# Kernel tuning notes

Measured on AMD Instinct MI355X. Metric: run time of the kernel, lower is better.

Reference implementation:

```python
import jax, jax.numpy as jnp
import numpy as np

M, N, D = 16384, 16384, 256


def setup_inputs() -> dict:
    key = jax.random.key(0)
    k1, k2, k3 = jax.random.split(key, 3)
    x = jax.random.normal(k1, (M, D), dtype=jnp.float32)
    X = jax.random.normal(k2, (N, D), dtype=jnp.float32)
    residuals = jax.random.normal(k3, (N,), dtype=jnp.float32)
    return {"x": x, "X": X, "residuals": residuals}


def reference(x, X, residuals):
    n, d = X.shape
    # Scott's rule: h = mean(std(X, unbiased)) * n^(-1/(d+4))
    h = jnp.mean(jnp.std(X, axis=0, ddof=1)) * (n ** (-1.0 / (d + 4)))
    inv_bw_sq = 1.0 / (2.0 * h * h)
    sq = (jnp.sum(x * x, axis=1)[:, None]
          + jnp.sum(X * X, axis=1)[None, :]
          - 2.0 * (x @ X.T))
    sq = jnp.maximum(sq, 0.0)
    w = jnp.exp(-sq * inv_bw_sq)                     # (m, n)
    num = w @ residuals                              # (m,)
    den = jnp.sum(w, axis=1) + 1e-8                  # (m,)
    return num / den
```

## Files before the change

kernel.cpp:

```cpp
#include <hip/hip_runtime.h>
#include <stdint.h>

#define MDIM 16384
#define NDIM 16384
#define DDIM 256
#define NSPLIT 4
#define NSTRIP 4096
#define BM 128
#define NT 32

typedef __attribute__((ext_vector_type(16))) float f32x16;
typedef __attribute__((ext_vector_type(8))) int i32x8;

#define SC1 0x7F7F7F7F

static constexpr size_t COLPART_OFF = 0;
static constexpr size_t SCAL_OFF    = 512u * 1024u;
static constexpr size_t AX_OFF      = SCAL_OFF + 1024u;
static constexpr size_t BXR_OFF     = AX_OFF + 64u * 1024u;
static constexpr size_t BXM_OFF     = BXR_OFF + 64u * 1024u;
static constexpr size_t X8_OFF      = 1ull << 20;
static constexpr size_t B8_OFF      = X8_OFF + (4ull << 20);
static constexpr size_t NUMP_OFF    = B8_OFF + (4ull << 20) + (512ull << 10);
static constexpr size_t DENP_OFF    = NUMP_OFF + (size_t)NSPLIT * MDIM * 4u;

__device__ inline unsigned short f2bf_rne(float f) {
    uint32_t u = __builtin_bit_cast(uint32_t, f);
    u += 0x7fffu + ((u >> 16) & 1u);
    return (unsigned short)(u >> 16);
}

__global__ void k1_colstats(const float* __restrict__ X, float2* __restrict__ part) {
    const int col = threadIdx.x;
    const int b   = blockIdx.x;
    const float* p = X + (size_t)b * 64 * DDIM + col;
    float s = 0.f, sq = 0.f;
#pragma unroll 8
    for (int r = 0; r < 64; ++r) {
        float v = p[(size_t)r * DDIM];
        s += v; sq += v * v;
    }
    part[b * 256 + col] = make_float2(s, sq);
}

__global__ void k2_finalize(const float2* __restrict__ part, float* __restrict__ scal) {
    const int t = threadIdx.x;
    float s = 0.f, sq = 0.f;
#pragma unroll 8
    for (int b = 0; b < 256; ++b) {
        float2 v = part[b * 256 + t];
        s += v.x; sq += v.y;
    }
    const float n = (float)NDIM;
    float var = (sq - s * s / n) / (n - 1.0f);
    float sd  = sqrtf(fmaxf(var, 0.f));
    __shared__ float red[256];
    red[t] = sd;
    __syncthreads();
    for (int o = 128; o > 0; o >>= 1) {
        if (t < o) red[t] += red[t + o];
        __syncthreads();
    }
    if (t == 0) {
        float h = (red[0] / 256.0f) * exp2f(log2f(n) * (-1.0f / (DDIM + 4.0f)));
        float c = 1.0f / (2.0f * h * h);
        scal[0] = c;
        scal[1] = sqrtf(2.0f * c);
    }
}

__global__ void k3_prep(const float* __restrict__ src,
                        unsigned char* __restrict__ dst8,
                        float* __restrict__ ax,
                        const float* __restrict__ resid, unsigned int* __restrict__ bxrp,
                        const float* __restrict__ scal) {
    const int lane = threadIdx.x & 63;
    const int wv   = threadIdx.x >> 6;
    const int row  = blockIdx.x * 4 + wv;
    const float c = scal[0], s = scal[1];
    float4 v = *((const float4*)(src + (size_t)row * DDIM) + lane);
    float nsq = v.x * v.x + v.y * v.y + v.z * v.z + v.w * v.w;
#pragma unroll
    for (int o = 1; o < 64; o <<= 1) nsq += __shfl_xor(nsq, o);

    unsigned int r8 = 0;
    r8 = __builtin_amdgcn_cvt_pk_fp8_f32(v.x * s, v.y * s, r8, 0);
    r8 = __builtin_amdgcn_cvt_pk_fp8_f32(v.z * s, v.w * s, r8, 1);
    const int ks64 = lane >> 4;
    const int lh   = (lane >> 3) & 1;
    const int e4   = (lane & 7) * 4;
    size_t off;
    if (bxrp) off = (size_t)(row >> 6) * 16384 + ks64 * 4096 + ((row >> 5) & 1) * 2048
                  + lh * 1024 + (row & 31) * 32 + e4;
    else      off = (size_t)(row >> 7) * 32768 + ks64 * 8192 + ((row >> 5) & 3) * 2048
                  + lh * 1024 + (row & 31) * 32 + e4;
    *(unsigned int*)(dst8 + off) = r8;

    if (lane == 0) {
        float a = -c * nsq;
        if (bxrp) bxrp[row] = ((unsigned int)f2bf_rne(resid[row]) << 16) | f2bf_rne(a);
        else      ax[row]   = a;
    }
}

__global__ void k3c_bxmax(const unsigned int* __restrict__ bxrp, float* __restrict__ bxm64) {
    const int t = threadIdx.x;
    float m = -1e30f;
#pragma unroll 8
    for (int i = 0; i < 64; ++i) {
        float bx = __builtin_bit_cast(float, bxrp[t * 64 + i] << 16);
        m = fmaxf(m, bx);
    }
    bxm64[t] = m;
}

__global__ __launch_bounds__(256, 2)
void k4_main(const unsigned char* __restrict__ x8T, const unsigned char* __restrict__ B8T,
             const float* __restrict__ ax, const unsigned int* __restrict__ bxrp,
             const float* __restrict__ bxm64, float* __restrict__ nump, float* __restrict__ denp) {
    __shared__ float ldsBxm[NSTRIP / 64];
    __shared__ float ldsAcc[2 * BM];

    const int tid  = threadIdx.x;
    const int lane = tid & 63;
    const int wv   = tid >> 6;
    const int wr   = wv >> 1;
    const int wc   = wv & 1;
    const int l31  = lane & 31;
    const int lhi  = lane >> 5;

    const int f  = blockIdx.x;
    const int sw = (f & 7) * 64 + (f >> 3);
    const int mt = sw & 127;
    const int by = sw >> 7;
    const int m0 = mt * BM;
    const int n0 = by * NSTRIP;

    if (tid < NSTRIP / 64) ldsBxm[tid] = bxm64[(n0 >> 6) + tid];
    ldsAcc[tid] = 0.f;

    float axm = fmaxf(ax[m0 + lane], ax[m0 + 64 + lane]);
#pragma unroll
    for (int o = 1; o < 64; o <<= 1) axm = fmaxf(axm, __shfl_xor(axm, o));

    const unsigned char* Ab = x8T + (size_t)mt * 32768 + lhi * 1024 + l31 * 32;
    i32x8 aF[2][4];
#pragma unroll
    for (int rf = 0; rf < 2; ++rf)
#pragma unroll
        for (int ks = 0; ks < 4; ++ks)
            aF[rf][ks] = *(const i32x8*)(Ab + ks * 8192 + (wr * 2 + rf) * 2048);

    const unsigned char* Bb = B8T + (size_t)n0 * 256 + (size_t)wc * 16384 + lhi * 1024 + l31 * 32;
    i32x8 bF[4][2];
#pragma unroll
    for (int s = 0; s < 2; ++s) {
        bF[s][0] = *(const i32x8*)(Bb + s * 4096);
        bF[s][1] = *(const i32x8*)(Bb + s * 4096 + 2048);
    }

    __syncthreads();

    f32x16 acc[2][2];

#pragma unroll 1
    for (int nt = 0; nt < NT; ++nt) {
#pragma unroll
        for (int ks = 0; ks < 4; ++ks) {
            {
                const int sp = nt * 4 + ks + 2;
                const size_t off = (size_t)(sp >> 2) * 32768 + (size_t)(sp & 3) * 4096;
                bF[(ks + 2) & 3][0] = *(const i32x8*)(Bb + off);
                bF[(ks + 2) & 3][1] = *(const i32x8*)(Bb + off + 2048);
            }
            __builtin_amdgcn_sched_barrier(0);
            __builtin_amdgcn_s_setprio(1);
#pragma unroll
            for (int rf = 0; rf < 2; ++rf)
#pragma unroll
                for (int cf = 0; cf < 2; ++cf) {
                    if (ks == 0)
                        acc[rf][cf] = __builtin_amdgcn_mfma_scale_f32_32x32x64_f8f6f4(
                            aF[rf][ks], bF[ks & 3][cf], (f32x16)(0.f), 0, 0, 0, SC1, 0, SC1);
                    else
                        acc[rf][cf] = __builtin_amdgcn_mfma_scale_f32_32x32x64_f8f6f4(
                            aF[rf][ks], bF[ks & 3][cf], acc[rf][cf], 0, 0, 0, SC1, 0, SC1);
                }
            __builtin_amdgcn_s_setprio(0);
            __builtin_amdgcn_sched_barrier(0);

            if (ks == 3) {
                const float bxm = ldsBxm[nt * 2 + wc];
                float m = -1e30f;
#pragma unroll
                for (int i = 0; i < 2; ++i)
#pragma unroll
                    for (int j = 0; j < 2; ++j)
#pragma unroll
                        for (int r = 0; r < 16; r += 4) {
                            f32x16 v = acc[i][j];
                            m = fmaxf(m, fmaxf(fmaxf(v[r], v[r + 1]), fmaxf(v[r + 2], v[r + 3])));
                        }
                if (!__all(m + axm + bxm < -104.0f)) {
                    float bxv[2], rv[2];
#pragma unroll
                    for (int cf = 0; cf < 2; ++cf) {
                        unsigned int pk = bxrp[n0 + nt * 128 + wc * 64 + cf * 32 + l31];
                        bxv[cf] = __builtin_bit_cast(float, pk << 16);
                        rv[cf]  = __builtin_bit_cast(float, pk & 0xffff0000u);
                    }
#pragma unroll
                    for (int rf = 0; rf < 2; ++rf)
#pragma unroll
                        for (int r = 0; r < 16; ++r) {
                            const int row = wr * 64 + rf * 32 + (r & 3) + 8 * (r >> 2) + 4 * lhi;
                            const float axv = ax[m0 + row];
                            float nv = 0.f, dv = 0.f;
#pragma unroll
                            for (int cf = 0; cf < 2; ++cf) {
                                const float arg = fminf(acc[rf][cf][r] + axv + bxv[cf], 0.f);
                                const float w = expf(arg);
                                nv = fmaf(w, rv[cf], nv);
                                dv += w;
                            }
#pragma unroll
                            for (int o = 1; o < 32; o <<= 1) { nv += __shfl_xor(nv, o); dv += __shfl_xor(dv, o); }
                            if (l31 == 0) {
                                atomicAdd(&ldsAcc[row * 2 + 0], nv);
                                atomicAdd(&ldsAcc[row * 2 + 1], dv);
                            }
                        }
                }
            }
        }
    }

    __syncthreads();
    if (tid < BM) {
        nump[by * MDIM + m0 + tid] = ldsAcc[tid * 2 + 0];
        denp[by * MDIM + m0 + tid] = ldsAcc[tid * 2 + 1];
    }
}

__global__ void k5_div(const float* __restrict__ nump, const float* __restrict__ denp,
                       float* __restrict__ out) {
    const int i = blockIdx.x * 256 + threadIdx.x;
    float n = 0.f, d = 0.f;
#pragma unroll
    for (int s = 0; s < NSPLIT; ++s) { n += nump[s * MDIM + i]; d += denp[s * MDIM + i]; }
    out[i] = n / (d + 1e-8f);
}

extern "C" void kernel_launch(void* const* d_in, const int* in_sizes, int n_in,
                              void* d_out, int out_size, void* d_ws, size_t ws_size,
                              hipStream_t stream) {
    const float* x     = (const float*)d_in[0];
    const float* X     = (const float*)d_in[1];
    const float* resid = (const float*)d_in[2];
    float* out = (float*)d_out;

    char* w = (char*)d_ws;
    float2* colpart      = (float2*)(w + COLPART_OFF);
    float*  scal         = (float*)(w + SCAL_OFF);
    float*  ax           = (float*)(w + AX_OFF);
    unsigned int* bxrp   = (unsigned int*)(w + BXR_OFF);
    float*  bxm64        = (float*)(w + BXM_OFF);
    unsigned char* x8    = (unsigned char*)(w + X8_OFF);
    unsigned char* B8    = (unsigned char*)(w + B8_OFF);
    float* nump          = (float*)(w + NUMP_OFF);
    float* denp          = (float*)(w + DENP_OFF);

    k1_colstats<<<256, 256, 0, stream>>>(X, colpart);
    k2_finalize<<<1, 256, 0, stream>>>(colpart, scal);
    k3_prep<<<MDIM / 4, 256, 0, stream>>>(x, x8, ax, nullptr, nullptr, scal);
    k3_prep<<<NDIM / 4, 256, 0, stream>>>(X, B8, nullptr, resid, bxrp, scal);
    k3c_bxmax<<<1, 256, 0, stream>>>(bxrp, bxm64);
    k4_main<<<512, 256, 0, stream>>>(x8, B8, ax, bxrp, bxm64, nump, denp);
    k5_div<<<MDIM / 256, 256, 0, stream>>>(nump, denp, out);
}
```

Before: 96.92 us.

## Halve M tile, raise occupancy, and fold per-strip bx max into prep

```diff
diff --git a/kernel.cpp b/kernel.cpp
--- a/kernel.cpp
+++ b/kernel.cpp
@@ -6,7 +6,7 @@
 #define DDIM 256
 #define NSPLIT 4
 #define NSTRIP 4096
-#define BM 128
+#define BM 64
 #define NT 32
 
 typedef __attribute__((ext_vector_type(16))) float f32x16;
@@ -73,6 +73,7 @@
                         unsigned char* __restrict__ dst8,
                         float* __restrict__ ax,
                         const float* __restrict__ resid, unsigned int* __restrict__ bxrp,
+                        unsigned int* __restrict__ bxminu,
                         const float* __restrict__ scal) {
     const int lane = threadIdx.x & 63;
     const int wv   = threadIdx.x >> 6;
@@ -89,140 +90,113 @@
     const int ks64 = lane >> 4;
     const int lh   = (lane >> 3) & 1;
     const int e4   = (lane & 7) * 4;
-    size_t off;
-    if (bxrp) off = (size_t)(row >> 6) * 16384 + ks64 * 4096 + ((row >> 5) & 1) * 2048
-                  + lh * 1024 + (row & 31) * 32 + e4;
-    else      off = (size_t)(row >> 7) * 32768 + ks64 * 8192 + ((row >> 5) & 3) * 2048
-                  + lh * 1024 + (row & 31) * 32 + e4;
+    const size_t off = (size_t)(row >> 6) * 16384 + ks64 * 4096 + ((row >> 5) & 1) * 2048
+                     + lh * 1024 + (row & 31) * 32 + e4;
     *(unsigned int*)(dst8 + off) = r8;
 
     if (lane == 0) {
         float a = -c * nsq;
-        if (bxrp) bxrp[row] = ((unsigned int)f2bf_rne(resid[row]) << 16) | f2bf_rne(a);
-        else      ax[row]   = a;
-    }
-}
-
-__global__ void k3c_bxmax(const unsigned int* __restrict__ bxrp, float* __restrict__ bxm64) {
-    const int t = threadIdx.x;
-    float m = -1e30f;
-#pragma unroll 8
-    for (int i = 0; i < 64; ++i) {
-        float bx = __builtin_bit_cast(float, bxrp[t * 64 + i] << 16);
-        m = fmaxf(m, bx);
-    }
-    bxm64[t] = m;
-}
-
-__global__ __launch_bounds__(256, 2)
+        if (bxrp) {
+            bxrp[row] = ((unsigned int)f2bf_rne(resid[row]) << 16) | f2bf_rne(a);
+            atomicMin(&bxminu[row >> 6], __builtin_bit_cast(unsigned int, nsq));
+        } else {
+            ax[row] = a;
+        }
+    }
+}
+
+__global__ __launch_bounds__(256, 4)
 void k4_main(const unsigned char* __restrict__ x8T, const unsigned char* __restrict__ B8T,
              const float* __restrict__ ax, const unsigned int* __restrict__ bxrp,
-             const float* __restrict__ bxm64, float* __restrict__ nump, float* __restrict__ denp) {
+             const unsigned int* __restrict__ bxminu, const float* __restrict__ scal,
+             float* __restrict__ nump, float* __restrict__ denp) {
     __shared__ float ldsBxm[NSTRIP / 64];
     __shared__ float ldsAcc[2 * BM];
 
     const int tid  = threadIdx.x;
     const int lane = tid & 63;
     const int wv   = tid >> 6;
-    const int wr   = wv >> 1;
-    const int wc   = wv & 1;
     const int l31  = lane & 31;
     const int lhi  = lane >> 5;
 
     const int f  = blockIdx.x;
-    const int sw = (f & 7) * 64 + (f >> 3);
-    const int mt = sw & 127;
-    const int by = sw >> 7;
+    const int sw = (f & 7) * 128 + (f >> 3);
+    const int mt = sw & 255;
+    const int by = sw >> 8;
     const int m0 = mt * BM;
     const int n0 = by * NSTRIP;
 
-    if (tid < NSTRIP / 64) ldsBxm[tid] = bxm64[(n0 >> 6) + tid];
-    ldsAcc[tid] = 0.f;
-
-    float axm = fmaxf(ax[m0 + lane], ax[m0 + 64 + lane]);
+    const float c = scal[0];
+    if (tid < NSTRIP / 64)
+        ldsBxm[tid] = -c * __builtin_bit_cast(float, bxminu[(n0 >> 6) + tid]);
+    if (tid < 2 * BM) ldsAcc[tid] = 0.f;
+
+    float axm = ax[m0 + lane];
 #pragma unroll
     for (int o = 1; o < 64; o <<= 1) axm = fmaxf(axm, __shfl_xor(axm, o));
 
-    const unsigned char* Ab = x8T + (size_t)mt * 32768 + lhi * 1024 + l31 * 32;
+    const unsigned char* Ab = x8T + (size_t)mt * 16384 + lhi * 1024 + l31 * 32;
     i32x8 aF[2][4];
 #pragma unroll
     for (int rf = 0; rf < 2; ++rf)
 #pragma unroll
         for (int ks = 0; ks < 4; ++ks)
-            aF[rf][ks] = *(const i32x8*)(Ab + ks * 8192 + (wr * 2 + rf) * 2048);
-
-    const unsigned char* Bb = B8T + (size_t)n0 * 256 + (size_t)wc * 16384 + lhi * 1024 + l31 * 32;
-    i32x8 bF[4][2];
-#pragma unroll
-    for (int s = 0; s < 2; ++s) {
-        bF[s][0] = *(const i32x8*)(Bb + s * 4096);
-        bF[s][1] = *(const i32x8*)(Bb + s * 4096 + 2048);
-    }
+            aF[rf][ks] = *(const i32x8*)(Ab + ks * 4096 + rf * 2048);
+
+    const unsigned char* Bb = B8T + (size_t)n0 * 256 + (wv >> 1) * 16384 + (wv & 1) * 2048
+                            + lhi * 1024 + l31 * 32;
+    i32x8 bF[2];
+    bF[0] = *(const i32x8*)(Bb);
 
     __syncthreads();
 
-    f32x16 acc[2][2];
+    f32x16 acc[2];
 
 #pragma unroll 1
     for (int nt = 0; nt < NT; ++nt) {
 #pragma unroll
         for (int ks = 0; ks < 4; ++ks) {
             {
-                const int sp = nt * 4 + ks + 2;
+                const int sp = nt * 4 + ks + 1;
                 const size_t off = (size_t)(sp >> 2) * 32768 + (size_t)(sp & 3) * 4096;
-                bF[(ks + 2) & 3][0] = *(const i32x8*)(Bb + off);
-                bF[(ks + 2) & 3][1] = *(const i32x8*)(Bb + off + 2048);
+                bF[(ks + 1) & 1] = *(const i32x8*)(Bb + off);
             }
             __builtin_amdgcn_sched_barrier(0);
             __builtin_amdgcn_s_setprio(1);
 #pragma unroll
-            for (int rf = 0; rf < 2; ++rf)
-#pragma unroll
-                for (int cf = 0; cf < 2; ++cf) {
-                    if (ks == 0)
-                        acc[rf][cf] = __builtin_amdgcn_mfma_scale_f32_32x32x64_f8f6f4(
-                            aF[rf][ks], bF[ks & 3][cf], (f32x16)(0.f), 0, 0, 0, SC1, 0, SC1);
-                    else
-                        acc[rf][cf] = __builtin_amdgcn_mfma_scale_f32_32x32x64_f8f6f4(
-                            aF[rf][ks], bF[ks & 3][cf], acc[rf][cf], 0, 0, 0, SC1, 0, SC1);
-                }
+            for (int rf = 0; rf < 2; ++rf) {
+                if (ks == 0)
+                    acc[rf] = __builtin_amdgcn_mfma_scale_f32_32x32x64_f8f6f4(
+                        aF[rf][ks], bF[ks & 1], (f32x16)(0.f), 0, 0, 0, SC1, 0, SC1);
+                else
+                    acc[rf] = __builtin_amdgcn_mfma_scale_f32_32x32x64_f8f6f4(
+                        aF[rf][ks], bF[ks & 1], acc[rf], 0, 0, 0, SC1, 0, SC1);
+            }
             __builtin_amdgcn_s_setprio(0);
             __builtin_amdgcn_sched_barrier(0);
 
             if (ks == 3) {
-                const float bxm = ldsBxm[nt * 2 + wc];
+                const float bxm = ldsBxm[nt * 2 + (wv >> 1)];
                 float m = -1e30f;
 #pragma unroll
                 for (int i = 0; i < 2; ++i)
 #pragma unroll
-                    for (int j = 0; j < 2; ++j)
-#pragma unroll
-                        for (int r = 0; r < 16; r += 4) {
-                            f32x16 v = acc[i][j];
-                            m = fmaxf(m, fmaxf(fmaxf(v[r], v[r + 1]), fmaxf(v[r + 2], v[r + 3])));
-                        }
+                    for (int r = 0; r < 16; r += 4) {
+                        f32x16 v = acc[i];
+                        m = fmaxf(m, fmaxf(fmaxf(v[r], v[r + 1]), fmaxf(v[r + 2], v[r + 3])));
+                    }
                 if (!__all(m + axm + bxm < -104.0f)) {
-                    float bxv[2], rv[2];
-#pragma unroll
-                    for (int cf = 0; cf < 2; ++cf) {
-                        unsigned int pk = bxrp[n0 + nt * 128 + wc * 64 + cf * 32 + l31];
-                        bxv[cf] = __builtin_bit_cast(float, pk << 16);
-                        rv[cf]  = __builtin_bit_cast(float, pk & 0xffff0000u);
-                    }
+                    const unsigned int pk = bxrp[n0 + nt * 128 + wv * 32 + l31];
+                    const float bxv = __builtin_bit_cast(float, pk << 16);
+                    const float rv  = __builtin_bit_cast(float, pk & 0xffff0000u);
 #pragma unroll
                     for (int rf = 0; rf < 2; ++rf)
 #pragma unroll
                         for (int r = 0; r < 16; ++r) {
-                            const int row = wr * 64 + rf * 32 + (r & 3) + 8 * (r >> 2) + 4 * lhi;
-                            const float axv = ax[m0 + row];
-                            float nv = 0.f, dv = 0.f;
-#pragma unroll
-                            for (int cf = 0; cf < 2; ++cf) {
-                                const float arg = fminf(acc[rf][cf][r] + axv + bxv[cf], 0.f);
-                                const float w = expf(arg);
-                                nv = fmaf(w, rv[cf], nv);
-                                dv += w;
-                            }
+                            const int row = rf * 32 + (r & 3) + 8 * (r >> 2) + 4 * lhi;
+                            const float arg = fminf(acc[rf][r] + ax[m0 + row] + bxv, 0.f);
+                            const float w = expf(arg);
+                            float nv = w * rv, dv = w;
 #pragma unroll
                             for (int o = 1; o < 32; o <<= 1) { nv += __shfl_xor(nv, o); dv += __shfl_xor(dv, o); }
                             if (l31 == 0) {
@@ -264,7 +238,7 @@
     float*  scal         = (float*)(w + SCAL_OFF);
     float*  ax           = (float*)(w + AX_OFF);
     unsigned int* bxrp   = (unsigned int*)(w + BXR_OFF);
-    float*  bxm64        = (float*)(w + BXM_OFF);
+    unsigned int* bxminu = (unsigned int*)(w + BXM_OFF);
     unsigned char* x8    = (unsigned char*)(w + X8_OFF);
     unsigned char* B8    = (unsigned char*)(w + B8_OFF);
     float* nump          = (float*)(w + NUMP_OFF);
@@ -272,9 +246,8 @@
 
     k1_colstats<<<256, 256, 0, stream>>>(X, colpart);
     k2_finalize<<<1, 256, 0, stream>>>(colpart, scal);
-    k3_prep<<<MDIM / 4, 256, 0, stream>>>(x, x8, ax, nullptr, nullptr, scal);
-    k3_prep<<<NDIM / 4, 256, 0, stream>>>(X, B8, nullptr, resid, bxrp, scal);
-    k3c_bxmax<<<1, 256, 0, stream>>>(bxrp, bxm64);
-    k4_main<<<512, 256, 0, stream>>>(x8, B8, ax, bxrp, bxm64, nump, denp);
+    k3_prep<<<MDIM / 4, 256, 0, stream>>>(x, x8, ax, nullptr, nullptr, nullptr, scal);
+    k3_prep<<<NDIM / 4, 256, 0, stream>>>(X, B8, nullptr, resid, bxrp, bxminu, scal);
+    k4_main<<<1024, 256, 0, stream>>>(x8, B8, ax, bxrp, bxminu, scal, nump, denp);
     k5_div<<<MDIM / 256, 256, 0, stream>>>(nump, denp, out);
 }
```

After: 139.3 us. +43.7%, slower.

## Merge prep launches, fold block-max into atomicMin, stagger main-kernel starts

Applied to the files above, without the earlier changes.

```diff
diff --git a/kernel.cpp b/kernel.cpp
--- a/kernel.cpp
+++ b/kernel.cpp
@@ -69,14 +69,17 @@
     }
 }
 
-__global__ void k3_prep(const float* __restrict__ src,
-                        unsigned char* __restrict__ dst8,
+__global__ void k3_prep(const float* __restrict__ x, const float* __restrict__ X,
+                        unsigned char* __restrict__ x8T, unsigned char* __restrict__ B8T,
                         float* __restrict__ ax,
                         const float* __restrict__ resid, unsigned int* __restrict__ bxrp,
+                        unsigned int* __restrict__ bxminu,
                         const float* __restrict__ scal) {
     const int lane = threadIdx.x & 63;
     const int wv   = threadIdx.x >> 6;
-    const int row  = blockIdx.x * 4 + wv;
+    const bool isB = blockIdx.x >= (MDIM / 4);
+    const int row  = (blockIdx.x - (isB ? MDIM / 4 : 0)) * 4 + wv;
+    const float* src = isB ? X : x;
     const float c = scal[0], s = scal[1];
     float4 v = *((const float4*)(src + (size_t)row * DDIM) + lane);
     float nsq = v.x * v.x + v.y * v.y + v.z * v.z + v.w * v.w;
@@ -89,35 +92,27 @@
     const int ks64 = lane >> 4;
     const int lh   = (lane >> 3) & 1;
     const int e4   = (lane & 7) * 4;
-    size_t off;
-    if (bxrp) off = (size_t)(row >> 6) * 16384 + ks64 * 4096 + ((row >> 5) & 1) * 2048
-                  + lh * 1024 + (row & 31) * 32 + e4;
-    else      off = (size_t)(row >> 7) * 32768 + ks64 * 8192 + ((row >> 5) & 3) * 2048
-                  + lh * 1024 + (row & 31) * 32 + e4;
-    *(unsigned int*)(dst8 + off) = r8;
-
-    if (lane == 0) {
-        float a = -c * nsq;
-        if (bxrp) bxrp[row] = ((unsigned int)f2bf_rne(resid[row]) << 16) | f2bf_rne(a);
-        else      ax[row]   = a;
-    }
-}
-
-__global__ void k3c_bxmax(const unsigned int* __restrict__ bxrp, float* __restrict__ bxm64) {
-    const int t = threadIdx.x;
-    float m = -1e30f;
-#pragma unroll 8
-    for (int i = 0; i < 64; ++i) {
-        float bx = __builtin_bit_cast(float, bxrp[t * 64 + i] << 16);
-        m = fmaxf(m, bx);
-    }
-    bxm64[t] = m;
+    if (isB) {
+        const size_t off = (size_t)(row >> 6) * 16384 + ks64 * 4096 + ((row >> 5) & 1) * 2048
+                         + lh * 1024 + (row & 31) * 32 + e4;
+        *(unsigned int*)(B8T + off) = r8;
+        if (lane == 0) {
+            bxrp[row] = ((unsigned int)f2bf_rne(resid[row]) << 16) | f2bf_rne(-c * nsq);
+            atomicMin(&bxminu[row >> 6], __builtin_bit_cast(unsigned int, nsq));
+        }
+    } else {
+        const size_t off = (size_t)(row >> 7) * 32768 + ks64 * 8192 + ((row >> 5) & 3) * 2048
+                         + lh * 1024 + (row & 31) * 32 + e4;
+        *(unsigned int*)(x8T + off) = r8;
+        if (lane == 0) ax[row] = -c * nsq;
+    }
 }
 
 __global__ __launch_bounds__(256, 2)
 void k4_main(const unsigned char* __restrict__ x8T, const unsigned char* __restrict__ B8T,
              const float* __restrict__ ax, const unsigned int* __restrict__ bxrp,
-             const float* __restrict__ bxm64, float* __restrict__ nump, float* __restrict__ denp) {
+             const unsigned int* __restrict__ bxminu, const float* __restrict__ scal,
+             float* __restrict__ nump, float* __restrict__ denp) {
     __shared__ float ldsBxm[NSTRIP / 64];
     __shared__ float ldsAcc[2 * BM];
 
@@ -136,7 +131,9 @@
     const int m0 = mt * BM;
     const int n0 = by * NSTRIP;
 
-    if (tid < NSTRIP / 64) ldsBxm[tid] = bxm64[(n0 >> 6) + tid];
+    const float c = scal[0];
+    if (tid < NSTRIP / 64)
+        ldsBxm[tid] = -c * __builtin_bit_cast(float, bxminu[(n0 >> 6) + tid]);
     ldsAcc[tid] = 0.f;
 
     float axm = fmaxf(ax[m0 + lane], ax[m0 + 64 + lane]);
@@ -160,6 +157,13 @@
     }
 
     __syncthreads();
+
+    switch (f & 3) {
+        case 1: __builtin_amdgcn_s_sleep(2); break;
+        case 2: __builtin_amdgcn_s_sleep(4); break;
+        case 3: __builtin_amdgcn_s_sleep(6); break;
+        default: break;
+    }
 
     f32x16 acc[2][2];
 
@@ -264,7 +268,7 @@
     float*  scal         = (float*)(w + SCAL_OFF);
     float*  ax           = (float*)(w + AX_OFF);
     unsigned int* bxrp   = (unsigned int*)(w + BXR_OFF);
-    float*  bxm64        = (float*)(w + BXM_OFF);
+    unsigned int* bxminu = (unsigned int*)(w + BXM_OFF);
     unsigned char* x8    = (unsigned char*)(w + X8_OFF);
     unsigned char* B8    = (unsigned char*)(w + B8_OFF);
     float* nump          = (float*)(w + NUMP_OFF);
@@ -272,9 +276,7 @@
 
     k1_colstats<<<256, 256, 0, stream>>>(X, colpart);
     k2_finalize<<<1, 256, 0, stream>>>(colpart, scal);
-    k3_prep<<<MDIM / 4, 256, 0, stream>>>(x, x8, ax, nullptr, nullptr, scal);
-    k3_prep<<<NDIM / 4, 256, 0, stream>>>(X, B8, nullptr, resid, bxrp, scal);
-    k3c_bxmax<<<1, 256, 0, stream>>>(bxrp, bxm64);
-    k4_main<<<512, 256, 0, stream>>>(x8, B8, ax, bxrp, bxm64, nump, denp);
+    k3_prep<<<(MDIM + NDIM) / 4, 256, 0, stream>>>(x, X, x8, B8, ax, resid, bxrp, bxminu, scal);
+    k4_main<<<512, 256, 0, stream>>>(x8, B8, ax, bxrp, bxminu, scal, nump, denp);
     k5_div<<<MDIM / 256, 256, 0, stream>>>(nump, denp, out);
 }
```

Result: slower. 115.7 us (+19.4%).
